# Optimization experiments

Hardware: AMD Instinct MI355X
Metric: run time of the kernel (lower is better)

## Reference

```python
import jax, jax.numpy as jnp
import numpy as np

B, S, E, H, W = 1, 4096, 1024, 16, 256
D = E // H
SCALE = D ** -0.5


def setup_inputs() -> dict:
    key = jax.random.key(0)
    k1, k2, k3 = jax.random.split(key, 3)
    x = jax.random.normal(k1, (B, S, E), dtype=jnp.float32)
    # torch Linear weight is [out,in]; we store transposed [in,out] so y = x @ w
    w_qkv = jax.random.normal(k2, (E, 3 * E), dtype=jnp.float32) * (E ** -0.5)
    w_out = jax.random.normal(k3, (E, E), dtype=jnp.float32) * (E ** -0.5)
    # sliding-window causal mask: key j allowed for query i iff i-W < j <= i
    q_idx = jnp.arange(S)[:, None]
    k_idx = jnp.arange(S)[None, :]
    allowed_mask = (k_idx <= q_idx) & (k_idx > q_idx - W)  # [S,S] bool
    allowed_mask = allowed_mask[None, None]  # [1,1,S,S]
    return {"x": x, "allowed_mask": allowed_mask, "w_qkv": w_qkv, "w_out": w_out}


def reference(x, allowed_mask, w_qkv, w_out):
    b, s, e = x.shape
    qkv = (x @ w_qkv).reshape(b, s, 3, H, D)
    q, k, v = jnp.moveaxis(qkv, 2, 0)  # each [b,s,H,D]
    q = q.transpose(0, 2, 1, 3)  # [b,H,s,D]
    k = k.transpose(0, 2, 1, 3)
    v = v.transpose(0, 2, 1, 3)
    scores = jnp.einsum('bhsd,bhtd->bhst', q, k) * SCALE  # [b,H,s,s]
    scores = jnp.where(allowed_mask, scores, -jnp.inf)
    attn = jax.nn.softmax(scores, axis=-1)
    out = jnp.einsum('bhst,bhtd->bhsd', attn, v)  # [b,H,s,D]
    out = out.transpose(0, 2, 1, 3).reshape(b, s, e)
    return out @ w_out
```

## Files before the change

kernel.cpp:

```cpp
#include <hip/hip_runtime.h>
#include <hip/hip_bf16.h>

#define S_LEN 4096
#define EMB   1024
#define NH    16
#define HD    64
#define WIN   256
#define SCALE 0.125f

typedef __attribute__((ext_vector_type(8))) short short8;
typedef __attribute__((ext_vector_type(4))) float f32x4;
typedef __attribute__((ext_vector_type(4))) unsigned short us4;

__device__ inline unsigned short f2b(float x) {
    __hip_bfloat16 b = __float2bfloat16(x);
    return *reinterpret_cast<unsigned short*>(&b);
}

__device__ inline void gld_lds16(const unsigned short* g, unsigned short* l) {
    __builtin_amdgcn_global_load_lds(
        (const __attribute__((address_space(1))) unsigned int*)g,
        (__attribute__((address_space(3))) unsigned int*)l,
        16, 0, 0);
}

__device__ inline void transpose_tile(const float* __restrict__ in,
                                      unsigned short* __restrict__ out,
                                      int R, int C, int bx, int by,
                                      unsigned short* t) {
    const int tid = threadIdx.x;
    const int r0 = by * 64, c0 = bx * 64;

    const int rr = tid >> 4, cc = (tid & 15) * 4;
    #pragma unroll
    for (int i = 0; i < 4; ++i) {
        float4 v = *reinterpret_cast<const float4*>(&in[(size_t)(r0 + rr + i * 16) * C + c0 + cc]);
        t[(cc + 0) * 72 + rr + i * 16] = f2b(v.x);
        t[(cc + 1) * 72 + rr + i * 16] = f2b(v.y);
        t[(cc + 2) * 72 + rr + i * 16] = f2b(v.z);
        t[(cc + 3) * 72 + rr + i * 16] = f2b(v.w);
    }
    __syncthreads();

    const int wr = tid >> 2, wk = (tid & 3) * 16;
    #pragma unroll
    for (int p = 0; p < 2; ++p)
        *reinterpret_cast<uint4*>(&out[(size_t)(c0 + wr) * R + r0 + wk + p * 8]) =
            *reinterpret_cast<const uint4*>(&t[wr * 72 + wk + p * 8]);
}

__global__ __launch_bounds__(256) void prep(const float* __restrict__ x,
                                            unsigned short* __restrict__ xb,
                                            const float* __restrict__ w_qkv,
                                            unsigned short* __restrict__ wqkvT,
                                            const float* __restrict__ w_out,
                                            unsigned short* __restrict__ woutT) {
    __shared__ alignas(16) unsigned short t[64 * 72];
    const int b = blockIdx.x;
    if (b < 768) {
        transpose_tile(w_qkv, wqkvT, EMB, 3 * EMB, b % 48, b / 48, t);
    } else if (b < 1024) {
        const int bb = b - 768;
        transpose_tile(w_out, woutT, EMB, EMB, bb & 15, bb >> 4, t);
    } else {
        const size_t tt = (size_t)(b - 1024) * 256 + threadIdx.x;
        const float4* s4 = reinterpret_cast<const float4*>(x) + tt * 4;
        float4 v0 = s4[0], v1 = s4[1], v2 = s4[2], v3 = s4[3];
        us4 p0 = {f2b(v0.x), f2b(v0.y), f2b(v0.z), f2b(v0.w)};
        us4 p1 = {f2b(v1.x), f2b(v1.y), f2b(v1.z), f2b(v1.w)};
        us4 p2 = {f2b(v2.x), f2b(v2.y), f2b(v2.z), f2b(v2.w)};
        us4 p3 = {f2b(v3.x), f2b(v3.y), f2b(v3.z), f2b(v3.w)};
        us4* d = reinterpret_cast<us4*>(xb) + tt * 4;
        d[0] = p0; d[1] = p1; d[2] = p2; d[3] = p3;
    }
}

template <int MODE, int BN>
__global__ __launch_bounds__(256) void gemm_bt(const unsigned short* __restrict__ A,
                                               const unsigned short* __restrict__ Bt,
                                               void* __restrict__ Cout,
                                               unsigned short* __restrict__ vT,
                                               int M, int N, int K) {
    constexpr int SMEM_ELEMS = (MODE == 1) ? 17408 : 8192 + BN * 64;
    constexpr int NJ = BN / 32;
    __shared__ alignas(16) unsigned short smem[SMEM_ELEMS];
    unsigned short* As = smem;
    unsigned short* Bs = smem + 8192;

    const int tid  = threadIdx.x;
    const int lane = tid & 63;
    const int w    = tid >> 6;
    const int quad = lane >> 4;
    const int l16  = lane & 15;

    const int m0 = blockIdx.y * 128;
    const int n0 = blockIdx.x * BN;
    const int m_off = (w & 1) * 64;
    const int n_off = (w >> 1) * (BN / 2);

    const int s_row = tid >> 3;
    const int s_c0  = tid & 7;

    f32x4 acc[4][NJ];
    #pragma unroll
    for (int i = 0; i < 4; ++i)
        #pragma unroll
        for (int j = 0; j < NJ; ++j)
            acc[i][j] = (f32x4){0.f, 0.f, 0.f, 0.f};

    for (int bk = 0; bk < K; bk += 64) {
        __syncthreads();
        #pragma unroll
        for (int p = 0; p < 4; ++p) {
            const int row = p * 32 + s_row;
            const int c   = s_c0 ^ (row & 7);
            gld_lds16(A + (size_t)(m0 + row) * K + bk + c * 8,
                      As + (p * 256 + w * 64) * 8);
        }
        #pragma unroll
        for (int p = 0; p < BN / 32; ++p) {
            const int row = p * 32 + s_row;
            const int c   = s_c0 ^ (row & 7);
            gld_lds16(Bt + (size_t)(n0 + row) * K + bk + c * 8,
                      Bs + (p * 256 + w * 64) * 8);
        }
        __syncthreads();

        #pragma unroll
        for (int ks = 0; ks < 2; ++ks) {
            short8 af[4], bf[NJ];
            #pragma unroll
            for (int i = 0; i < 4; ++i) {
                const int r = m_off + i * 16 + l16;
                af[i] = *reinterpret_cast<const short8*>(
                    &As[r * 64 + ((ks * 4 + quad) ^ (r & 7)) * 8]);
            }
            #pragma unroll
            for (int j = 0; j < NJ; ++j) {
                const int r = n_off + j * 16 + l16;
                bf[j] = *reinterpret_cast<const short8*>(
                    &Bs[r * 64 + ((ks * 4 + quad) ^ (r & 7)) * 8]);
            }
            #pragma unroll
            for (int i = 0; i < 4; ++i)
                #pragma unroll
                for (int j = 0; j < NJ; ++j)
                    acc[i][j] = __builtin_amdgcn_mfma_f32_16x16x32_bf16(
                        af[i], bf[j], acc[i][j], 0, 0, 0);
        }
    }

    if (MODE == 0) {
        float* C = (float*)Cout;
        #pragma unroll
        for (int i = 0; i < 4; ++i)
            #pragma unroll
            for (int r = 0; r < 4; ++r) {
                const size_t row = m0 + m_off + i * 16 + quad * 4 + r;
                #pragma unroll
                for (int j = 0; j < NJ; ++j)
                    C[row * N + n0 + n_off + j * 16 + l16] = acc[i][j][r];
            }
    } else if (n0 < 2048) {
        const float sc = (n0 < 1024) ? SCALE : 1.0f;
        unsigned short* C = (unsigned short*)Cout;
        #pragma unroll
        for (int i = 0; i < 4; ++i)
            #pragma unroll
            for (int r = 0; r < 4; ++r) {
                const size_t row = m0 + m_off + i * 16 + quad * 4 + r;
                #pragma unroll
                for (int j = 0; j < NJ; ++j)
                    C[row * N + n0 + n_off + j * 16 + l16] = f2b(acc[i][j][r] * sc);
            }
    } else {
        __syncthreads();
        #pragma unroll
        for (int i = 0; i < 4; ++i) {
            const int ss = m_off + i * 16 + quad * 4;
            #pragma unroll
            for (int j = 0; j < NJ; ++j) {
                const int dd = n_off + j * 16 + l16;
                us4 pk = {f2b(acc[i][j][0]), f2b(acc[i][j][1]),
                          f2b(acc[i][j][2]), f2b(acc[i][j][3])};
                *reinterpret_cast<us4*>(&smem[dd * 136 + ss]) = pk;
            }
        }
        __syncthreads();
        #pragma unroll
        for (int p = 0; p < 8; ++p) {
            const int t  = p * 256 + tid;
            const int dd = t >> 4;
            const int sc2 = (t & 15) * 8;
            *reinterpret_cast<uint4*>(&vT[(size_t)(n0 - 2048 + dd) * S_LEN + m0 + sc2]) =
                *reinterpret_cast<const uint4*>(&smem[dd * 136 + sc2]);
        }
    }
}

__global__ __launch_bounds__(512) void gemm_qkv(const unsigned short* __restrict__ A,
                                                const unsigned short* __restrict__ Bt,
                                                unsigned short* __restrict__ C,
                                                unsigned short* __restrict__ vT) {
    __shared__ alignas(16) unsigned short smem[65536];

    constexpr int K = EMB;
    const int tid  = threadIdx.x;
    const int lane = tid & 63;
    const int w    = tid >> 6;
    const int quad = lane >> 4;
    const int l16  = lane & 15;
    const int wr   = w >> 2, wc = w & 3;
    const int wm0  = wr * 128, wn0 = wc * 64;

    const int raw = blockIdx.x;
    const int s   = (raw & 7) * 24 + (raw >> 3);
    const int by  = s / 12, bx = s % 12;
    const int m0  = by * 256, n0 = bx * 256;

    const int srow = tid >> 2;
    const int scp  = tid & 3;
    const int sc4  = scp ^ ((srow >> 1) & 3);
    const unsigned short* pA = A  + (size_t)(m0 + srow) * K + sc4 * 8;
    const unsigned short* pB = Bt + (size_t)(n0 + srow) * K + sc4 * 8;
    const int dls = (w * 64) * 8;

    auto STAGE = [&](int q) {
        unsigned short* dA = smem + ((q >> 1) & 1) * 32768 + (q & 1) * 8192 + dls;
        unsigned short* dB = dA + 16384;
        const int gk = q * 32;
        gld_lds16(pA + gk, dA);
        gld_lds16(pA + (size_t)128 * K + gk, dA + 4096);
        gld_lds16(pB + gk, dB);
        gld_lds16(pB + (size_t)128 * K + gk, dB + 4096);
    };

    const int cpf = quad ^ ((l16 >> 1) & 3);
    const int oA  = (wm0 + l16) * 32 + cpf * 8;
    const int oB  = (wn0 + l16) * 32 + cpf * 8;

    f32x4 acc[8][4];
    #pragma unroll
    for (int i = 0; i < 8; ++i)
        #pragma unroll
        for (int j = 0; j < 4; ++j)
            acc[i][j] = (f32x4){0.f, 0.f, 0.f, 0.f};

    auto PHASE = [&](int p, bool stage_ok) {
        const unsigned short* Ab = smem + ((p >> 1) & 1) * 32768 + (p & 1) * 8192;
        const unsigned short* Bb = Ab + 16384;
        short8 af[8], bf[4];
        #pragma unroll
        for (int i = 0; i < 8; ++i)
            af[i] = *reinterpret_cast<const short8*>(&Ab[oA + i * 512]);
        #pragma unroll
        for (int j = 0; j < 4; ++j)
            bf[j] = *reinterpret_cast<const short8*>(&Bb[oB + j * 512]);
        if (stage_ok) STAGE(p + 3);
        __builtin_amdgcn_sched_barrier(0);
        __builtin_amdgcn_s_setprio(1);
        #pragma unroll
        for (int i = 0; i < 8; ++i)
            #pragma unroll
            for (int j = 0; j < 4; ++j)
                acc[i][j] = __builtin_amdgcn_mfma_f32_16x16x32_bf16(af[i], bf[j], acc[i][j], 0, 0, 0);
        __builtin_amdgcn_s_setprio(0);
    };

    STAGE(0); STAGE(1); STAGE(2);
    asm volatile("s_waitcnt vmcnt(8)" ::: "memory");
    __builtin_amdgcn_s_barrier();

    for (int pp = 0; pp < 28; pp += 4) {
        #pragma unroll
        for (int e = 0; e < 4; ++e) {
            PHASE(pp + e, true);
            asm volatile("s_waitcnt vmcnt(8)" ::: "memory");
            __builtin_amdgcn_s_barrier();
        }
    }
    PHASE(28, true);
    asm volatile("s_waitcnt vmcnt(8)" ::: "memory");
    __builtin_amdgcn_s_barrier();
    PHASE(29, false);
    asm volatile("s_waitcnt vmcnt(4)" ::: "memory");
    __builtin_amdgcn_s_barrier();
    PHASE(30, false);
    asm volatile("s_waitcnt vmcnt(0)" ::: "memory");
    __builtin_amdgcn_s_barrier();
    PHASE(31, false);
    __builtin_amdgcn_s_barrier();

    const int sec = n0 >> 10;
    if (sec < 2) {
        const float sc = (sec == 0) ? SCALE : 1.0f;
        #pragma unroll
        for (int i = 0; i < 8; ++i) {
            #pragma unroll
            for (int r = 0; r < 4; ++r) {
                const size_t row = (size_t)(m0 + wm0 + i * 16 + quad * 4 + r) * 3072;
                #pragma unroll
                for (int j = 0; j < 4; ++j)
                    C[row + n0 + wn0 + j * 16 + l16] = f2b(acc[i][j][r] * sc);
            }
        }
    } else {
        #pragma unroll
        for (int i = 0; i < 8; ++i) {
            const int ss = wm0 + i * 16 + quad * 4;
            const int sc0 = ss >> 3, se = ss & 7;
            #pragma unroll
            for (int j = 0; j < 4; ++j) {
                const int d = wn0 + j * 16 + l16;
                us4 pk = {f2b(acc[i][j][0]), f2b(acc[i][j][1]),
                          f2b(acc[i][j][2]), f2b(acc[i][j][3])};
                *reinterpret_cast<us4*>(&smem[d * 256 + ((sc0 ^ (d & 31)) << 3) + se]) = pk;
            }
        }
        __builtin_amdgcn_s_barrier();
        const int vb = n0 - 2048;
        #pragma unroll
        for (int rep = 0; rep < 16; ++rep) {
            const int idx = rep * 512 + tid;
            const int d = idx >> 5, scr = idx & 31;
            *reinterpret_cast<uint4*>(&vT[(size_t)(vb + d) * S_LEN + m0 + scr * 8]) =
                *reinterpret_cast<const uint4*>(&smem[d * 256 + ((scr ^ (d & 31)) << 3)]);
        }
    }
}

__global__ __launch_bounds__(256) void attn_mfma(const unsigned short* __restrict__ qkv,
                                                 const unsigned short* __restrict__ vT,
                                                 unsigned short* __restrict__ outb) {
    __shared__ alignas(16) unsigned short lds[40960];
    unsigned short* KtP = lds;
    unsigned short* Vt  = lds + 20480;

    const int raw  = blockIdx.x + (blockIdx.y << 6);
    const int xcd  = raw & 7;
    const int slot = raw >> 3;
    const int q0   = (xcd * 8 + (slot & 7)) * 64;
    const int h    = slot >> 3;

    const int tid  = threadIdx.x;
    const int w    = tid >> 6;
    const int lane = tid & 63;
    const int quad = lane >> 4;
    const int l16  = lane & 15;
    const int kbase = q0 - 256;

    const unsigned short* qrow = qkv + (size_t)(q0 + w * 16 + l16) * 3072 + h * 64;
    short8 aq[2];
    aq[0] = *reinterpret_cast<const short8*>(qrow + quad * 8);
    aq[1] = *reinterpret_cast<const short8*>(qrow + 32 + quad * 8);

    #pragma unroll
    for (int i = 0; i < 10; ++i) {
        const int fc  = i * 256 + tid;
        const int row = fc >> 3, p = fc & 7;
        const int c   = p ^ (row & 7);
        int j = kbase + row; if (j < 0) j = 0;
        gld_lds16(qkv + (size_t)j * 3072 + EMB + h * 64 + c * 8,
                  KtP + (i * 256 + w * 64) * 8);
    }

    __syncthreads();

    #pragma unroll
    for (int i = 0; i < 10; ++i) {
        const int fc = i * 256 + tid;
        const int d  = fc / 40, pp = fc % 40;
        const int cc = (pp & ~7) | ((pp & 7) ^ (d & 7));
        int j0 = kbase + cc * 8; if (j0 < 0) j0 = 0;
        gld_lds16(vT + (size_t)(h * 64 + d) * S_LEN + j0,
                  Vt + (i * 256 + w * 64) * 8);
    }

    f32x4 accs[17];
    #pragma unroll
    for (int nb = 0; nb < 17; ++nb) accs[nb] = (f32x4){0.f, 0.f, 0.f, 0.f};

    #pragma unroll
    for (int ks = 0; ks < 2; ++ks)
        #pragma unroll
        for (int nb = 0; nb < 17; ++nb) {
            const int row = (w + nb) * 16 + l16;
            const int p   = (ks * 4 + quad) ^ (l16 & 7);
            const short8 bfr = *reinterpret_cast<const short8*>(&KtP[row * 64 + p * 8]);
            accs[nb] = __builtin_amdgcn_mfma_f32_16x16x32_bf16(aq[ks], bfr, accs[nb], 0, 0, 0);
        }

    __syncthreads();

    const int i0 = q0 + w * 16 + quad * 4;
    const int rw0 = w * 16 + quad * 4;
    float rsum[4] = {0.f, 0.f, 0.f, 0.f};
    #pragma unroll
    for (int nb = 0; nb < 17; ++nb) {
        const int t   = w + nb;
        const int j   = kbase + t * 16 + l16;
        const int cch = (t * 16 + l16) >> 3, e = l16 & 7;
        #pragma unroll
        for (int r = 0; r < 4; ++r) {
            const int i = i0 + r;
            const bool ok = (j >= 0) & (j <= i) & (j > i - WIN);
            const float ev = ok ? __expf(accs[nb][r]) : 0.f;
            rsum[r] += ev;
            const int rw  = rw0 + r;
            const int pos = (cch & ~7) | ((cch & 7) ^ (rw & 7));
            KtP[rw * 320 + pos * 8 + e] = f2b(ev);
        }
    }
    {
        const int tz = (w & 1) ? (w - 1) : (w + 17);
        const int cch = (tz * 16 + l16) >> 3, e = l16 & 7;
        #pragma unroll
        for (int r = 0; r < 4; ++r) {
            const int rw  = rw0 + r;
            const int pos = (cch & ~7) | ((cch & 7) ^ (rw & 7));
            KtP[rw * 320 + pos * 8 + e] = 0;
        }
    }
    float inv[4];
    #pragma unroll
    for (int r = 0; r < 4; ++r) {
        float s = rsum[r];
        #pragma unroll
        for (int off = 1; off < 16; off <<= 1)
            s += __shfl_xor(s, off, 64);
        inv[r] = 1.f / s;
    }

    f32x4 acco[4];
    #pragma unroll
    for (int nb2 = 0; nb2 < 4; ++nb2) acco[nb2] = (f32x4){0.f, 0.f, 0.f, 0.f};

    const int ks0 = w >> 1;
    #pragma unroll
    for (int ksi = 0; ksi < 9; ++ksi) {
        const int ks   = ks0 + ksi;
        const int prow = w * 16 + l16;
        const int cc   = ks * 4 + quad;
        const int ppos = (cc & ~7) | ((cc & 7) ^ (prow & 7));
        const short8 af = *reinterpret_cast<const short8*>(&KtP[prow * 320 + ppos * 8]);
        #pragma unroll
        for (int nb2 = 0; nb2 < 4; ++nb2) {
            const int d    = nb2 * 16 + l16;
            const int vpos = (cc & ~7) | ((cc & 7) ^ (d & 7));
            const short8 bfr = *reinterpret_cast<const short8*>(&Vt[d * 320 + vpos * 8]);
            acco[nb2] = __builtin_amdgcn_mfma_f32_16x16x32_bf16(af, bfr, acco[nb2], 0, 0, 0);
        }
    }

    #pragma unroll
    for (int nb2 = 0; nb2 < 4; ++nb2)
        #pragma unroll
        for (int r = 0; r < 4; ++r)
            outb[(size_t)(q0 + w * 16 + quad * 4 + r) * EMB + h * 64 + nb2 * 16 + l16] =
                f2b(acco[nb2][r] * inv[r]);
}

extern "C" void kernel_launch(void* const* d_in, const int* in_sizes, int n_in,
                              void* d_out, int out_size, void* d_ws, size_t ws_size,
                              hipStream_t stream) {
    const float* x     = (const float*)d_in[0];
    const float* w_qkv = (const float*)d_in[2];
    const float* w_out = (const float*)d_in[3];
    float* out = (float*)d_out;

    char* ws = (char*)d_ws;
    unsigned short* xb     = (unsigned short*)(ws);
    unsigned short* wqkvT  = (unsigned short*)(ws + (8u  << 20));
    unsigned short* woutT  = (unsigned short*)(ws + (14u << 20));
    unsigned short* qkvb   = (unsigned short*)(ws + (16u << 20));
    unsigned short* attnb  = (unsigned short*)(ws + (48u << 20));
    unsigned short* vT     = (unsigned short*)(ws + (56u << 20));

    prep<<<2048, 256, 0, stream>>>(x, xb, w_qkv, wqkvT, w_out, woutT);

    gemm_qkv<<<dim3(192), 512, 0, stream>>>(xb, wqkvT, qkvb, vT);

    attn_mfma<<<dim3(S_LEN / 64, NH), 256, 0, stream>>>(qkvb, vT, attnb);

    gemm_bt<0, 64><<<dim3(EMB / 64, S_LEN / 128), 256, 0, stream>>>(
        attnb, woutT, out, nullptr, S_LEN, EMB, EMB);
}
```

Baseline: 184.4 us.

## Load V fragments directly from global into registers, halve attention LDS

The attention kernel no longer stages the transposed V tile into LDS. Each lane now loads its V MFMA operands straight from global memory into double-buffered registers, prefetching one k-step ahead, which cuts LDS use in half and may allow more resident blocks per CU. The cost is more global-load traffic and latency exposed inside the PV loop, with redundant loads across waves. Separately, a sched_barrier in the GEMM phase is removed, which lets the compiler interleave the staging loads with the MFMAs.

```diff
diff --git a/kernel.cpp b/kernel.cpp
--- a/kernel.cpp
+++ b/kernel.cpp
@@ -257,7 +257,6 @@
         for (int j = 0; j < 4; ++j)
             bf[j] = *reinterpret_cast<const short8*>(&Bb[oB + j * 512]);
         if (stage_ok) STAGE(p + 3);
-        __builtin_amdgcn_sched_barrier(0);
         __builtin_amdgcn_s_setprio(1);
         #pragma unroll
         for (int i = 0; i < 8; ++i)
@@ -332,9 +331,7 @@
 __global__ __launch_bounds__(256) void attn_mfma(const unsigned short* __restrict__ qkv,
                                                  const unsigned short* __restrict__ vT,
                                                  unsigned short* __restrict__ outb) {
-    __shared__ alignas(16) unsigned short lds[40960];
-    unsigned short* KtP = lds;
-    unsigned short* Vt  = lds + 20480;
+    __shared__ alignas(16) unsigned short KtP[20480];
 
     const int raw  = blockIdx.x + (blockIdx.y << 6);
     const int xcd  = raw & 7;
@@ -366,16 +363,6 @@
 
     __syncthreads();
 
-    #pragma unroll
-    for (int i = 0; i < 10; ++i) {
-        const int fc = i * 256 + tid;
-        const int d  = fc / 40, pp = fc % 40;
-        const int cc = (pp & ~7) | ((pp & 7) ^ (d & 7));
-        int j0 = kbase + cc * 8; if (j0 < 0) j0 = 0;
-        gld_lds16(vT + (size_t)(h * 64 + d) * S_LEN + j0,
-                  Vt + (i * 256 + w * 64) * 8);
-    }
-
     f32x4 accs[17];
     #pragma unroll
     for (int nb = 0; nb < 17; ++nb) accs[nb] = (f32x4){0.f, 0.f, 0.f, 0.f};
@@ -391,6 +378,17 @@
         }
 
     __syncthreads();
+
+    const int ks0 = w >> 1;
+    const unsigned short* vb0 = vT + (size_t)(h * 64 + l16) * S_LEN;
+    short8 vfA[4], vfB[4];
+    {
+        int jj = kbase + (ks0 * 4 + quad) * 8;
+        if (jj < 0) jj = 0;
+        #pragma unroll
+        for (int n = 0; n < 4; ++n)
+            vfA[n] = *reinterpret_cast<const short8*>(vb0 + (size_t)n * 16 * S_LEN + jj);
+    }
 
     const int i0 = q0 + w * 16 + quad * 4;
     const int rw0 = w * 16 + quad * 4;
@@ -435,21 +433,30 @@
     #pragma unroll
     for (int nb2 = 0; nb2 < 4; ++nb2) acco[nb2] = (f32x4){0.f, 0.f, 0.f, 0.f};
 
-    const int ks0 = w >> 1;
+    const int prow = w * 16 + l16;
     #pragma unroll
     for (int ksi = 0; ksi < 9; ++ksi) {
-        const int ks   = ks0 + ksi;
-        const int prow = w * 16 + l16;
+        const int ks = ks0 + ksi;
+        if (ksi < 8) {
+            int jj = kbase + ((ks + 1) * 4 + quad) * 8;
+            if (jj < 0) jj = 0;
+            if ((ksi & 1) == 0) {
+                #pragma unroll
+                for (int n = 0; n < 4; ++n)
+                    vfB[n] = *reinterpret_cast<const short8*>(vb0 + (size_t)n * 16 * S_LEN + jj);
+            } else {
+                #pragma unroll
+                for (int n = 0; n < 4; ++n)
+                    vfA[n] = *reinterpret_cast<const short8*>(vb0 + (size_t)n * 16 * S_LEN + jj);
+            }
+        }
         const int cc   = ks * 4 + quad;
         const int ppos = (cc & ~7) | ((cc & 7) ^ (prow & 7));
         const short8 af = *reinterpret_cast<const short8*>(&KtP[prow * 320 + ppos * 8]);
         #pragma unroll
-        for (int nb2 = 0; nb2 < 4; ++nb2) {
-            const int d    = nb2 * 16 + l16;
-            const int vpos = (cc & ~7) | ((cc & 7) ^ (d & 7));
-            const short8 bfr = *reinterpret_cast<const short8*>(&Vt[d * 320 + vpos * 8]);
-            acco[nb2] = __builtin_amdgcn_mfma_f32_16x16x32_bf16(af, bfr, acco[nb2], 0, 0, 0);
-        }
+        for (int nb2 = 0; nb2 < 4; ++nb2)
+            acco[nb2] = __builtin_amdgcn_mfma_f32_16x16x32_bf16(
+                af, ((ksi & 1) == 0) ? vfA[nb2] : vfB[nb2], acco[nb2], 0, 0, 0);
     }
 
     #pragma unroll
```

Result: slower. 194.1 us (+5.3%).

## Compute transposed QK^T so P stays in registers; stage through small per-wave LDS scratch

Applied to the files above, without the earlier changes.

The attention kernel now computes K·Q^T so each lane holds scores for its own query row. That lets the row sum be reduced with two shuffles, and the bf16 probabilities are packed in registers instead of written as a full P tile to LDS. During PV, P fragments are streamed through a small double-buffered per-wave scratch, which shrinks LDS from 80KB to 52KB and sets launch_bounds(256,3) for higher occupancy. A sched_barrier is also dropped in the GEMM phase, and the register pressure from keeping 17 packed P fragments per lane may cause spills.

```diff
diff --git a/kernel.cpp b/kernel.cpp
--- a/kernel.cpp
+++ b/kernel.cpp
@@ -257,7 +257,6 @@
         for (int j = 0; j < 4; ++j)
             bf[j] = *reinterpret_cast<const short8*>(&Bb[oB + j * 512]);
         if (stage_ok) STAGE(p + 3);
-        __builtin_amdgcn_sched_barrier(0);
         __builtin_amdgcn_s_setprio(1);
         #pragma unroll
         for (int i = 0; i < 8; ++i)
@@ -329,12 +328,45 @@
     }
 }
 
-__global__ __launch_bounds__(256) void attn_mfma(const unsigned short* __restrict__ qkv,
-                                                 const unsigned short* __restrict__ vT,
-                                                 unsigned short* __restrict__ outb) {
-    __shared__ alignas(16) unsigned short lds[40960];
-    unsigned short* KtP = lds;
-    unsigned short* Vt  = lds + 20480;
+typedef __attribute__((ext_vector_type(2))) unsigned int u32x2;
+
+template <int PAR>
+__device__ __forceinline__ void pv_phase(const u32x2 (&PA)[17], unsigned short* scrw,
+                                         const unsigned short* Vt, f32x4 (&acco)[4],
+                                         int ks0, int quad, int l16, short8 af) {
+    const int wq  = quad & 1;
+    const int tlq = quad >> 1;
+    #pragma unroll
+    for (int ksi = 0; ksi < 9; ++ksi) {
+        const int ks = ks0 + ksi;
+        if (ksi < 8) {
+            #pragma unroll
+            for (int tl = 0; tl < 2; ++tl) {
+                const int nb = 2 * (ksi + 1) + tl - PAR;
+                u32x2 v = (nb >= 0 && nb <= 16) ? PA[(nb < 0) ? 0 : ((nb > 16) ? 16 : nb)]
+                                                : (u32x2){0u, 0u};
+                *reinterpret_cast<u32x2*>(&scrw[((ksi + 1) & 1) * 768 + tl * 384 + l16 * 24 + quad * 4]) = v;
+            }
+        }
+        const int cc = ks * 4 + quad;
+        #pragma unroll
+        for (int nb2 = 0; nb2 < 4; ++nb2) {
+            const int d    = nb2 * 16 + l16;
+            const int vpos = (cc & ~7) | ((cc & 7) ^ (d & 7));
+            const short8 bfr = *reinterpret_cast<const short8*>(&Vt[d * 320 + vpos * 8]);
+            acco[nb2] = __builtin_amdgcn_mfma_f32_16x16x32_bf16(af, bfr, acco[nb2], 0, 0, 0);
+        }
+        if (ksi < 8)
+            af = *reinterpret_cast<const short8*>(&scrw[((ksi + 1) & 1) * 768 + tlq * 384 + l16 * 24 + wq * 8]);
+    }
+}
+
+__global__ __launch_bounds__(256, 3) void attn_mfma(const unsigned short* __restrict__ qkv,
+                                                    const unsigned short* __restrict__ vT,
+                                                    unsigned short* __restrict__ outb) {
+    __shared__ alignas(16) unsigned short lds[26624];
+    unsigned short* KtV = lds;
+    unsigned short* scr = lds + 20480;
 
     const int raw  = blockIdx.x + (blockIdx.y << 6);
     const int xcd  = raw & 7;
@@ -361,8 +393,40 @@
         const int c   = p ^ (row & 7);
         int j = kbase + row; if (j < 0) j = 0;
         gld_lds16(qkv + (size_t)j * 3072 + EMB + h * 64 + c * 8,
-                  KtP + (i * 256 + w * 64) * 8);
-    }
+                  KtV + (i * 256 + w * 64) * 8);
+    }
+
+    __syncthreads();
+
+    const int iq = q0 + w * 16 + l16;
+    float rsum = 0.f;
+    u32x2 PA[17];
+    #pragma unroll
+    for (int nb = 0; nb < 17; ++nb) {
+        const int row = (w + nb) * 16 + l16;
+        f32x4 acc = (f32x4){0.f, 0.f, 0.f, 0.f};
+        #pragma unroll
+        for (int ks = 0; ks < 2; ++ks) {
+            const int p = (ks * 4 + quad) ^ (l16 & 7);
+            const short8 kf = *reinterpret_cast<const short8*>(&KtV[row * 64 + p * 8]);
+            acc = __builtin_amdgcn_mfma_f32_16x16x32_bf16(kf, aq[ks], acc, 0, 0, 0);
+        }
+        const int jb = kbase + (w + nb) * 16 + quad * 4;
+        float ev0, ev1, ev2, ev3;
+        {
+            const int j0 = jb, j1 = jb + 1, j2 = jb + 2, j3 = jb + 3;
+            ev0 = ((j0 >= 0) & (j0 <= iq) & (j0 > iq - WIN)) ? __expf(acc[0]) : 0.f;
+            ev1 = ((j1 >= 0) & (j1 <= iq) & (j1 > iq - WIN)) ? __expf(acc[1]) : 0.f;
+            ev2 = ((j2 >= 0) & (j2 <= iq) & (j2 > iq - WIN)) ? __expf(acc[2]) : 0.f;
+            ev3 = ((j3 >= 0) & (j3 <= iq) & (j3 > iq - WIN)) ? __expf(acc[3]) : 0.f;
+        }
+        rsum += (ev0 + ev1) + (ev2 + ev3);
+        PA[nb][0] = ((unsigned)f2b(ev1) << 16) | f2b(ev0);
+        PA[nb][1] = ((unsigned)f2b(ev3) << 16) | f2b(ev2);
+    }
+    rsum += __shfl_xor(rsum, 16, 64);
+    rsum += __shfl_xor(rsum, 32, 64);
+    const float inv_l = 1.f / rsum;
 
     __syncthreads();
 
@@ -373,91 +437,42 @@
         const int cc = (pp & ~7) | ((pp & 7) ^ (d & 7));
         int j0 = kbase + cc * 8; if (j0 < 0) j0 = 0;
         gld_lds16(vT + (size_t)(h * 64 + d) * S_LEN + j0,
-                  Vt + (i * 256 + w * 64) * 8);
-    }
-
-    f32x4 accs[17];
-    #pragma unroll
-    for (int nb = 0; nb < 17; ++nb) accs[nb] = (f32x4){0.f, 0.f, 0.f, 0.f};
-
-    #pragma unroll
-    for (int ks = 0; ks < 2; ++ks)
-        #pragma unroll
-        for (int nb = 0; nb < 17; ++nb) {
-            const int row = (w + nb) * 16 + l16;
-            const int p   = (ks * 4 + quad) ^ (l16 & 7);
-            const short8 bfr = *reinterpret_cast<const short8*>(&KtP[row * 64 + p * 8]);
-            accs[nb] = __builtin_amdgcn_mfma_f32_16x16x32_bf16(aq[ks], bfr, accs[nb], 0, 0, 0);
-        }
+                  KtV + (i * 256 + w * 64) * 8);
+    }
+
+    unsigned short* scrw = scr + w * 1536;
+    const int par = w & 1;
+    {
+        const u32x2 z = {0u, 0u};
+        u32x2 v0 = par ? z : PA[0];
+        u32x2 v1 = par ? PA[0] : PA[1];
+        *reinterpret_cast<u32x2*>(&scrw[0 * 384 + l16 * 24 + quad * 4]) = v0;
+        *reinterpret_cast<u32x2*>(&scrw[1 * 384 + l16 * 24 + quad * 4]) = v1;
+    }
+    const short8 af0 = *reinterpret_cast<const short8*>(
+        &scrw[(quad >> 1) * 384 + l16 * 24 + (quad & 1) * 8]);
 
     __syncthreads();
 
-    const int i0 = q0 + w * 16 + quad * 4;
-    const int rw0 = w * 16 + quad * 4;
-    float rsum[4] = {0.f, 0.f, 0.f, 0.f};
-    #pragma unroll
-    for (int nb = 0; nb < 17; ++nb) {
-        const int t   = w + nb;
-        const int j   = kbase + t * 16 + l16;
-        const int cch = (t * 16 + l16) >> 3, e = l16 & 7;
-        #pragma unroll
-        for (int r = 0; r < 4; ++r) {
-            const int i = i0 + r;
-            const bool ok = (j >= 0) & (j <= i) & (j > i - WIN);
-            const float ev = ok ? __expf(accs[nb][r]) : 0.f;
-            rsum[r] += ev;
-            const int rw  = rw0 + r;
-            const int pos = (cch & ~7) | ((cch & 7) ^ (rw & 7));
-            KtP[rw * 320 + pos * 8 + e] = f2b(ev);
-        }
-    }
-    {
-        const int tz = (w & 1) ? (w - 1) : (w + 17);
-        const int cch = (tz * 16 + l16) >> 3, e = l16 & 7;
-        #pragma unroll
-        for (int r = 0; r < 4; ++r) {
-            const int rw  = rw0 + r;
-            const int pos = (cch & ~7) | ((cch & 7) ^ (rw & 7));
-            KtP[rw * 320 + pos * 8 + e] = 0;
-        }
-    }
-    float inv[4];
-    #pragma unroll
-    for (int r = 0; r < 4; ++r) {
-        float s = rsum[r];
-        #pragma unroll
-        for (int off = 1; off < 16; off <<= 1)
-            s += __shfl_xor(s, off, 64);
-        inv[r] = 1.f / s;
-    }
-
     f32x4 acco[4];
     #pragma unroll
     for (int nb2 = 0; nb2 < 4; ++nb2) acco[nb2] = (f32x4){0.f, 0.f, 0.f, 0.f};
 
     const int ks0 = w >> 1;
-    #pragma unroll
-    for (int ksi = 0; ksi < 9; ++ksi) {
-        const int ks   = ks0 + ksi;
-        const int prow = w * 16 + l16;
-        const int cc   = ks * 4 + quad;
-        const int ppos = (cc & ~7) | ((cc & 7) ^ (prow & 7));
-        const short8 af = *reinterpret_cast<const short8*>(&KtP[prow * 320 + ppos * 8]);
-        #pragma unroll
-        for (int nb2 = 0; nb2 < 4; ++nb2) {
-            const int d    = nb2 * 16 + l16;
-            const int vpos = (cc & ~7) | ((cc & 7) ^ (d & 7));
-            const short8 bfr = *reinterpret_cast<const short8*>(&Vt[d * 320 + vpos * 8]);
-            acco[nb2] = __builtin_amdgcn_mfma_f32_16x16x32_bf16(af, bfr, acco[nb2], 0, 0, 0);
-        }
-    }
+    if (par == 0) pv_phase<0>(PA, scrw, KtV, acco, ks0, quad, l16, af0);
+    else          pv_phase<1>(PA, scrw, KtV, acco, ks0, quad, l16, af0);
+
+    float invo[4];
+    #pragma unroll
+    for (int r = 0; r < 4; ++r)
+        invo[r] = __shfl(inv_l, quad * 4 + r, 64);
 
     #pragma unroll
     for (int nb2 = 0; nb2 < 4; ++nb2)
         #pragma unroll
         for (int r = 0; r < 4; ++r)
             outb[(size_t)(q0 + w * 16 + quad * 4 + r) * EMB + h * 64 + nb2 * 16 + l16] =
-                f2b(acco[nb2][r] * inv[r]);
+                f2b(acco[nb2][r] * invo[r]);
 }
 
 extern "C" void kernel_launch(void* const* d_in, const int* in_sizes, int n_in,
```

Result: no change. 182.0 us (-1.3%).
